# Kernel optimization log

Hardware: AMD Instinct MI355X
Metric: run time of the kernel (lower is better)

## Reference

```python
import jax, jax.numpy as jnp
import numpy as np

BS, C, H, W = 16, 192, 120, 120
AN = 36            # agent_num
KS = 3             # kernel_size
POOL = 6           # int(sqrt(agent_num))
MID = 2 * AN // 4  # 18
EPS = 1e-5


def _conv(x, w, groups=1):
    return jax.lax.conv_general_dilated(
        x, w, window_strides=(1, 1), padding='SAME',
        dimension_numbers=('NCHW', 'OIHW', 'NCHW'),
        feature_group_count=groups)


def _bn(x, g, b, m, v):
    # inference-mode BatchNorm2d with running stats
    inv = g / jnp.sqrt(v + EPS)
    return x * inv[None, :, None, None] + (b - m * inv)[None, :, None, None]


def _pool6(x):
    # AdaptiveAvgPool2d(6) with H,W divisible by 6 == exact average pooling
    bs, c, h, w = x.shape
    return x.reshape(bs, c, POOL, h // POOL, POOL, w // POOL).mean(axis=(3, 5))


def setup_inputs() -> dict:
    key = jax.random.key(0)
    ks = jax.random.split(key, 14)
    u = lambda k, s: jax.random.uniform(k, s, jnp.float32, 0.5, 1.5)
    n = lambda k, s, sc: jax.random.normal(k, s, jnp.float32) * sc
    return {
        'x':      n(ks[0], (BS, C, H, W), 1.0),
        'key_w':  n(ks[1], (C, C // 3, KS, KS), 0.05),   # grouped conv, groups=3
        'bn1_g':  u(ks[2], (C,)),
        'bn1_b':  n(ks[3], (C,), 0.1),
        'bn1_m':  n(ks[4], (C,), 0.1),
        'bn1_v':  u(ks[5], (C,)),
        'val_w':  n(ks[6], (C, C, 1, 1), 0.05),
        'att_w1': n(ks[7], (MID, 2 * AN, 1, 1), 0.1),
        'bn2_g':  u(ks[8], (MID,)),
        'bn2_b':  n(ks[9], (MID,), 0.1),
        'bn2_m':  n(ks[10], (MID,), 0.1),
        'bn2_v':  u(ks[11], (MID,)),
        'att_w2': n(ks[12], (KS * KS * AN, MID, 1, 1), 0.1),
        'att_b2': n(ks[13], (KS * KS * AN,), 0.1),
    }


def reference(x, key_w, bn1_g, bn1_b, bn1_m, bn1_v, val_w,
              att_w1, bn2_g, bn2_b, bn2_m, bn2_v, att_w2, att_b2):
    bs, c, h, w = x.shape
    hw = h * w
    # key embedding: grouped conv -> BN -> ReLU
    k1 = jax.nn.relu(_bn(_conv(x, key_w, groups=3), bn1_g, bn1_b, bn1_m, bn1_v))
    # agent tokens and pooled values (torch .view semantics: raw row-major reshape)
    agent = _pool6(x).reshape(bs, AN, c)                 # (bs, 36, c)  channel-mixed view
    v = _pool6(_conv(x, val_w)).reshape(bs, c, AN)       # (bs, c, 36)
    k1r = k1.reshape(bs, hw, c)                          # torch k1.view(bs,-1,c)
    q1 = x.reshape(bs, hw, c)
    # agent<->key and query<->agent attention
    agent_attn = jax.nn.softmax(jnp.einsum('bac,bnc->ban', agent, k1r), axis=-1)  # (bs,36,hw)
    q_attn = jax.nn.softmax(jnp.einsum('bnc,bac->bna', q1, agent), axis=-1)       # (bs,hw,36)
    y = jnp.concatenate([agent_attn, jnp.swapaxes(q_attn, 1, 2)], axis=1)          # (bs,72,hw)
    y = y.reshape(bs, 2 * AN, h, w)
    # conv-generated attention map
    t = jax.nn.relu(_bn(_conv(y, att_w1), bn2_g, bn2_b, bn2_m, bn2_v))
    att = _conv(t, att_w2) + att_b2[None, :, None, None]                           # (bs,324,h,w)
    att = att.reshape(bs, AN, KS * KS, h, w).mean(axis=2).reshape(bs, hw, AN)
    k2 = jax.nn.softmax(att, axis=-1)                                              # (bs,hw,36)
    k2v = jnp.einsum('bna,bca->bnc', k2, v)                                        # (bs,hw,c)
    out = jnp.swapaxes(k2v, 1, 2).reshape(bs, c, h, w) + k1
    return out
```

## Files before the change

kernel.cpp:

```cpp
#include <hip/hip_runtime.h>
#include <hip/hip_bf16.h>
#include <math.h>

#define BS 16
#define C 192
#define H 120
#define W 120
#define HW 14400
#define AN 36
#define MID 18
#define CPG 64
#define EPS 1e-5f
#define SPX 128
#define BPS 200
#define NWQ 13824
#define XROWS 122
#define XCOLS 132
#define OPX 64
#define WST 72

typedef __attribute__((ext_vector_type(8))) short s16x8;
typedef __attribute__((ext_vector_type(4))) float f32x4;
typedef __attribute__((ext_vector_type(4))) unsigned short u16x4;

static __device__ __forceinline__ short f2bf(float f) {
    union { float f; unsigned u; } v; v.f = f;
    unsigned r = (v.u + 0x7FFF + ((v.u >> 16) & 1)) >> 16;
    return (short)r;
}
static __device__ __forceinline__ float bf2f(unsigned short u) {
    union { unsigned u; float f; } v; v.u = ((unsigned)u) << 16;
    return v.f;
}
static __device__ __forceinline__ s16x8 cvt8(float4 f0, float4 f1) {
    s16x8 v;
    v[0] = f2bf(f0.x); v[1] = f2bf(f0.y); v[2] = f2bf(f0.z); v[3] = f2bf(f0.w);
    v[4] = f2bf(f1.x); v[5] = f2bf(f1.y); v[6] = f2bf(f1.z); v[7] = f2bf(f1.w);
    return v;
}

__global__ __launch_bounds__(256) void k_wfold(const float* __restrict__ kw,
                                               const float* __restrict__ g1,
                                               const float* __restrict__ v1,
                                               unsigned short* __restrict__ Wq) {
    int u = blockIdx.x * 256 + threadIdx.x;
    if (u >= NWQ) return;
    int gc = u / 2304, rem = u - gc * 2304;
    int g = gc >> 1, cc = gc & 1;
    int th = rem >> 6, co = rem & 63;
    int tap = th >> 2, hi = th & 3;
    int cog = g * 64 + co;
    float inv = g1[cog] * rsqrtf(v1[cog] + EPS);
    const float* wp = kw + ((size_t)cog * 64 + cc * 32 + hi * 8) * 9 + tap;
    s16x8 v;
    #pragma unroll
    for (int e = 0; e < 8; ++e) v[e] = f2bf(wp[e * 9] * inv);
    *(s16x8*)&Wq[(size_t)u * 8] = v;
}

__global__ __launch_bounds__(256) void k_xt(const float* __restrict__ x,
                                            unsigned short* __restrict__ xTp) {
    int y = blockIdx.x, b = blockIdx.y;
    int t = threadIdx.x;
    __shared__ unsigned short L[120 * 200];
    for (int u = t; u < 24 * 120; u += 256) {
        int oc = u / 120, px = u - oc * 120;
        const float* xp = x + ((size_t)b * C + oc * 8) * HW + y * W + px;
        s16x8 v;
        #pragma unroll
        for (int j = 0; j < 8; ++j) v[j] = f2bf(xp[(size_t)j * HW]);
        *(s16x8*)&L[px * 200 + oc * 8] = v;
    }
    __syncthreads();
    for (int u = t; u < 24 * XCOLS; u += 256) {
        int oc = u / XCOLS, p = u - oc * XCOLS;
        int px = p - 1;
        s16x8 v = {0, 0, 0, 0, 0, 0, 0, 0};
        if (px >= 0 && px < 120) v = *(const s16x8*)&L[px * 200 + oc * 8];
        *(s16x8*)&xTp[(((size_t)(b * 24 + oc)) * XROWS + (y + 1)) * XCOLS * 8 + p * 8] = v;
    }
    if (y == 0 || y == H - 1) {
        int r = (y == 0) ? 0 : XROWS - 1;
        s16x8 z = {0, 0, 0, 0, 0, 0, 0, 0};
        for (int u = t; u < 24 * XCOLS; u += 256) {
            int oc = u / XCOLS, p = u - oc * XCOLS;
            *(s16x8*)&xTp[(((size_t)(b * 24 + oc)) * XROWS + r) * XCOLS * 8 + p * 8] = z;
        }
    }
}

__global__ __launch_bounds__(256) void k_pool(const float* __restrict__ x,
                                              float* __restrict__ P) {
    int bc = blockIdx.x;
    const float* xp = x + (size_t)bc * HW;
    __shared__ float acc[AN];
    int tid = threadIdx.x;
    if (tid < AN) acc[tid] = 0.f;
    __syncthreads();
    for (int s = tid; s < 720; s += 256) {
        int y = s / 6, xs = s % 6;
        const float4* p4 = (const float4*)(xp + y * W + xs * 20);
        float sum = 0.f;
        #pragma unroll
        for (int i = 0; i < 5; ++i) {
            float4 v = p4[i];
            sum += v.x + v.y + v.z + v.w;
        }
        atomicAdd(&acc[(y / 20) * 6 + xs], sum);
    }
    __syncthreads();
    if (tid < AN) P[(size_t)bc * AN + tid] = acc[tid] * (1.f / 400.f);
}

__global__ __launch_bounds__(256) void k_val(const float* __restrict__ valw,
                                             const float* __restrict__ P,
                                             unsigned short* __restrict__ Vb) {
    int b = blockIdx.x;
    __shared__ float Pl[C * AN];
    int tid = threadIdx.x;
    for (int i = tid; i < C * AN; i += 256) Pl[i] = P[(size_t)b * C * AN + i];
    __syncthreads();
    for (int o = tid; o < C * 8; o += 256) {
        int cc = o >> 3, a8 = o & 7;
        s16x8 vv = {0, 0, 0, 0, 0, 0, 0, 0};
        #pragma unroll
        for (int j = 0; j < 8; ++j) {
            int a = a8 * 8 + j;
            if (a < AN) {
                float s = 0.f;
                for (int k = 0; k < C; ++k) s += valw[cc * C + k] * Pl[k * AN + a];
                vv[j] = f2bf(s);
            }
        }
        *(s16x8*)&Vb[((size_t)b * C + cc) * 64 + a8 * 8] = vv;
    }
}

__global__ __launch_bounds__(256, 4) void k_conv_mfma(
        const unsigned short* __restrict__ xTp, const unsigned short* __restrict__ Wq,
        const float* __restrict__ g1, const float* __restrict__ b1,
        const float* __restrict__ m1, const float* __restrict__ v1,
        float* __restrict__ k1f, unsigned short* __restrict__ k1b, int writeF32) {
    int yp = blockIdx.x, g = blockIdx.y, b = blockIdx.z;
    int y0 = yp * 2;
    int t = threadIdx.x;
    __shared__ short xl[(2048 + 2) * 8];

    int w = t >> 6, l = t & 63, lr = l & 15, hi = l >> 4;
    int ry = w >> 1, xh = w & 1;
    f32x4 acc[4][4];
    #pragma unroll
    for (int mt = 0; mt < 4; ++mt)
        #pragma unroll
        for (int nt = 0; nt < 4; ++nt)
            acc[mt][nt] = (f32x4){0.f, 0.f, 0.f, 0.f};

    for (int cc = 0; cc < 2; ++cc) {
        if (cc) __syncthreads();
        const unsigned short* xbase =
            xTp + ((size_t)((b * 24 + g * 8 + cc * 4) * XROWS) + y0) * XCOLS * 8;
        #pragma unroll
        for (int k = 0; k < 8; ++k) {
            int u = t + 256 * k;
            int run = u >> 7, p = u & 127;
            int oct = run >> 2, r = run & 3;
            s16x8 v = *(const s16x8*)&xbase[((size_t)(oct * XROWS + r)) * XCOLS * 8 + p * 8];
            *(s16x8*)&xl[u * 8] = v;
        }
        __syncthreads();
        const s16x8* wq = (const s16x8*)Wq + (size_t)(g * 2 + cc) * 2304;
        s16x8 Bn[4];
        #pragma unroll
        for (int nt = 0; nt < 4; ++nt) Bn[nt] = wq[hi * 64 + nt * 16 + lr];
        #pragma unroll
        for (int tap = 0; tap < 9; ++tap) {
            int ky = tap / 3, kx = tap % 3;
            s16x8 Bc[4];
            #pragma unroll
            for (int nt = 0; nt < 4; ++nt) Bc[nt] = Bn[nt];
            if (tap < 8) {
                #pragma unroll
                for (int nt = 0; nt < 4; ++nt)
                    Bn[nt] = wq[((tap + 1) * 4 + hi) * 64 + nt * 16 + lr];
            }
            s16x8 A[4];
            #pragma unroll
            for (int mt = 0; mt < 4; ++mt) {
                int col = xh * 64 + mt * 16 + lr + kx;
                A[mt] = *(const s16x8*)&xl[((hi * 4 + ry + ky) * 128 + col) * 8];
            }
            #pragma unroll
            for (int mt = 0; mt < 4; ++mt)
                #pragma unroll
                for (int nt = 0; nt < 4; ++nt)
                    acc[mt][nt] = __builtin_amdgcn_mfma_f32_16x16x32_bf16(
                        A[mt], Bc[nt], acc[mt][nt], 0, 0, 0);
        }
    }
    int y = y0 + ry;
    #pragma unroll
    for (int nt = 0; nt < 4; ++nt) {
        int cog = g * CPG + nt * 16 + lr;
        float inv = g1[cog] * rsqrtf(v1[cog] + EPS);
        float beta = b1[cog] - m1[cog] * inv;
        #pragma unroll
        for (int mt = 0; mt < 4; ++mt) {
            int xcol = xh * 64 + mt * 16 + hi * 4;
            if (xcol >= 120) continue;
            float r0 = fmaxf(acc[mt][nt][0] + beta, 0.f);
            float r1 = fmaxf(acc[mt][nt][1] + beta, 0.f);
            float r2 = fmaxf(acc[mt][nt][2] + beta, 0.f);
            float r3 = fmaxf(acc[mt][nt][3] + beta, 0.f);
            size_t base = ((size_t)(b * C + cog)) * HW + y * W + xcol;
            if (writeF32) {
                *(float4*)&k1f[base] = make_float4(r0, r1, r2, r3);
            } else {
                u16x4 q;
                q[0] = (unsigned short)f2bf(r0); q[1] = (unsigned short)f2bf(r1);
                q[2] = (unsigned short)f2bf(r2); q[3] = (unsigned short)f2bf(r3);
                *(u16x4*)&k1b[base] = q;
            }
        }
    }
}

__global__ __launch_bounds__(256, 3) void k_scores_mfma(
        const float* __restrict__ Pp, const float* __restrict__ k1f,
        const unsigned short* __restrict__ k1b, const float* __restrict__ x,
        const unsigned short* __restrict__ xTp,
        float* __restrict__ S1, float* __restrict__ S2) {
    int b = blockIdx.y;
    int n0 = blockIdx.x * SPX;
    int t = threadIdx.x;
    int w = t >> 6, l = t & 63, lr = l & 15, hi = l >> 4;
    __shared__ short Bp[SPX * BPS];

    s16x8 afr[3][6];
    const float* ab = Pp + (size_t)b * (C * AN);
    #pragma unroll
    for (int mt = 0; mt < 3; ++mt) {
        int row = mt * 16 + lr;
        #pragma unroll
        for (int kc = 0; kc < 6; ++kc) {
            s16x8 v = {0, 0, 0, 0, 0, 0, 0, 0};
            if (row < AN) {
                const float4* ap = (const float4*)(ab + row * C + kc * 32 + hi * 8);
                v = cvt8(ap[0], ap[1]);
            }
            afr[mt][kc] = v;
        }
    }

    #pragma unroll 1
    for (int s = 0; s < 2; ++s) {
        __syncthreads();
        if (s == 0 && k1b) {
            const unsigned short* src = k1b + (size_t)b * C * HW + (size_t)n0 * C;
            for (int i = t; i < SPX * 24; i += 256) {
                int row = i / 24, o = i - row * 24;
                s16x8 v = {0, 0, 0, 0, 0, 0, 0, 0};
                if (n0 + row < HW) v = *(const s16x8*)&src[row * C + o * 8];
                *(s16x8*)&Bp[row * BPS + o * 8] = v;
            }
        } else if (s == 1 && xTp) {
            for (int i = t; i < SPX * 24; i += 256) {
                int row = i / 24, oc = i - row * 24;
                int n = n0 + row;
                s16x8 v = {0, 0, 0, 0, 0, 0, 0, 0};
                if (n < HW) {
                    int yy = n / 120, xx = n - yy * 120;
                    v = *(const s16x8*)&xTp[(((size_t)(b * 24 + oc)) * XROWS + yy + 1) *
                                            XCOLS * 8 + (xx + 1) * 8];
                }
                *(s16x8*)&Bp[row * BPS + oc * 8] = v;
            }
        } else {
            const float* sf = (s == 0) ? k1f : x;
            const float4* src = (const float4*)(sf + (size_t)b * C * HW + (size_t)n0 * C);
            for (int i = t; i < SPX * 24; i += 256) {
                int row = i / 24, c8 = (i - row * 24) * 8;
                s16x8 v = {0, 0, 0, 0, 0, 0, 0, 0};
                if (n0 + row < HW)
                    v = cvt8(src[row * 48 + c8 / 4], src[row * 48 + c8 / 4 + 1]);
                *(s16x8*)&Bp[row * BPS + c8] = v;
            }
        }
        __syncthreads();
        f32x4 acc[3][2];
        #pragma unroll
        for (int mt = 0; mt < 3; ++mt)
            #pragma unroll
            for (int pt = 0; pt < 2; ++pt)
                acc[mt][pt] = (f32x4){0.f, 0.f, 0.f, 0.f};
        #pragma unroll
        for (int kc = 0; kc < 6; ++kc) {
            s16x8 bf[2];
            #pragma unroll
            for (int pt = 0; pt < 2; ++pt) {
                int px = (w * 2 + pt) * 16 + lr;
                bf[pt] = *(const s16x8*)&Bp[px * BPS + kc * 32 + hi * 8];
            }
            #pragma unroll
            for (int mt = 0; mt < 3; ++mt)
                #pragma unroll
                for (int pt = 0; pt < 2; ++pt)
                    acc[mt][pt] = __builtin_amdgcn_mfma_f32_16x16x32_bf16(
                        afr[mt][kc], bf[pt], acc[mt][pt], 0, 0, 0);
        }
        float* dst = (s == 0 ? S1 : S2) + (size_t)b * AN * HW + n0;
        #pragma unroll
        for (int mt = 0; mt < 3; ++mt)
            #pragma unroll
            for (int pt = 0; pt < 2; ++pt) {
                int px = (w * 2 + pt) * 16 + lr;
                if (n0 + px >= HW) continue;
                #pragma unroll
                for (int r = 0; r < 4; ++r) {
                    int a = mt * 16 + hi * 4 + r;
                    if (a < AN) dst[(size_t)a * HW + px] = acc[mt][pt][r];
                }
            }
    }
}

__global__ __launch_bounds__(256) void k_rowstats(const float* __restrict__ S,
                                                  float* __restrict__ stats) {
    int row = blockIdx.x;
    const float* p = S + (size_t)row * HW;
    int tid = threadIdx.x;
    __shared__ float red[4];
    float m = -1e30f;
    for (int i = tid; i < HW / 4; i += 256) {
        float4 v = ((const float4*)p)[i];
        m = fmaxf(m, fmaxf(fmaxf(v.x, v.y), fmaxf(v.z, v.w)));
    }
    #pragma unroll
    for (int off = 32; off > 0; off >>= 1) m = fmaxf(m, __shfl_down(m, off, 64));
    if ((tid & 63) == 0) red[tid >> 6] = m;
    __syncthreads();
    m = fmaxf(fmaxf(red[0], red[1]), fmaxf(red[2], red[3]));
    __syncthreads();
    float s = 0.f;
    for (int i = tid; i < HW / 4; i += 256) {
        float4 v = ((const float4*)p)[i];
        s += __expf(v.x - m) + __expf(v.y - m) + __expf(v.z - m) + __expf(v.w - m);
    }
    #pragma unroll
    for (int off = 32; off > 0; off >>= 1) s += __shfl_down(s, off, 64);
    if ((tid & 63) == 0) red[tid >> 6] = s;
    __syncthreads();
    if (tid == 0) {
        stats[row] = m;
        stats[576 + row] = 1.f / (red[0] + red[1] + red[2] + red[3]);
    }
}

__global__ __launch_bounds__(256) void k_fuse(const float* __restrict__ A1,
                                              const float* __restrict__ stats,
                                              const float* __restrict__ S2,
                                              const float* __restrict__ w1,
                                              const float* __restrict__ g2,
                                              const float* __restrict__ b2,
                                              const float* __restrict__ m2,
                                              const float* __restrict__ v2,
                                              const float* __restrict__ w2,
                                              const float* __restrict__ bias2,
                                              float* __restrict__ AM) {
    int b = blockIdx.y;
    int tid = threadIdx.x;
    int N = blockIdx.x * 256 + tid;
    __shared__ float W1f[MID * 72];
    __shared__ float b1f[MID];
    __shared__ float W2m[AN * MID];
    __shared__ float b2m[AN];
    __shared__ float sm_m[AN], sm_ri[AN];
    for (int i = tid; i < MID * 72; i += 256) {
        int m = i / 72;
        W1f[i] = w1[i] * (g2[m] * rsqrtf(v2[m] + EPS));
    }
    if (tid < MID) {
        float inv = g2[tid] * rsqrtf(v2[tid] + EPS);
        b1f[tid] = b2[tid] - m2[tid] * inv;
    }
    for (int i = tid; i < AN * MID; i += 256) {
        int a = i / MID, m = i % MID;
        float s = 0.f;
        #pragma unroll
        for (int k = 0; k < 9; ++k) s += w2[(a * 9 + k) * MID + m];
        W2m[i] = s * (1.f / 9.f);
    }
    if (tid < AN) {
        float s = 0.f;
        #pragma unroll
        for (int k = 0; k < 9; ++k) s += bias2[tid * 9 + k];
        b2m[tid] = s * (1.f / 9.f);
        sm_m[tid] = stats[b * AN + tid];
        sm_ri[tid] = stats[576 + b * AN + tid];
    }
    __syncthreads();
    if (N >= HW) return;
    float yv[72];
    const float* a1p = A1 + (size_t)b * AN * HW + N;
    #pragma unroll
    for (int j = 0; j < AN; ++j)
        yv[j] = __expf(a1p[(size_t)j * HW] - sm_m[j]) * sm_ri[j];
    const float* s2p = S2 + (size_t)b * AN * HW + N;
    float mx = -1e30f;
    #pragma unroll
    for (int j = 0; j < AN; ++j) {
        float v = s2p[(size_t)j * HW];
        yv[AN + j] = v;
        mx = fmaxf(mx, v);
    }
    float ssum = 0.f;
    #pragma unroll
    for (int j = 0; j < AN; ++j) {
        float e = __expf(yv[AN + j] - mx);
        yv[AN + j] = e;
        ssum += e;
    }
    float rs = 1.f / ssum;
    #pragma unroll
    for (int j = 0; j < AN; ++j) yv[AN + j] *= rs;
    float t[MID];
    #pragma unroll
    for (int m = 0; m < MID; ++m) {
        float a = b1f[m];
        #pragma unroll
        for (int j = 0; j < 72; ++j) a += W1f[m * 72 + j] * yv[j];
        t[m] = a > 0.f ? a : 0.f;
    }
    float* amp = AM + (size_t)b * AN * HW + N;
    #pragma unroll
    for (int a = 0; a < AN; ++a) {
        float acc = b2m[a];
        #pragma unroll
        for (int m = 0; m < MID; ++m) acc += W2m[a * MID + m] * t[m];
        amp[(size_t)a * HW] = acc;
    }
}

__global__ __launch_bounds__(256) void k_out_mfma(const float* __restrict__ AM,
                                                  const unsigned short* __restrict__ Vb,
                                                  const unsigned short* __restrict__ k1b,
                                                  float* __restrict__ outp) {
    int b = blockIdx.y;
    int N0 = blockIdx.x * OPX;
    int t = threadIdx.x;
    __shared__ short wl[OPX * WST];

    {
        int p = t >> 2, q = t & 3;
        int N = N0 + p;
        int a = N / 400;
        int n0w = (N - a * 400) * AN;
        const float* amp = AM + ((size_t)b * AN + a) * HW + n0w;
        const int qoff = (q == 0) ? 0 : (q == 1) ? 12 : (q == 2) ? 20 : 32;
        const int qn4 = (q == 0) ? 3 : (q == 1) ? 2 : (q == 2) ? 3 : 1;
        float vals[12];
        const float4* ap = (const float4*)(amp + qoff);
        #pragma unroll
        for (int i = 0; i < 3; ++i) {
            if (i < qn4) {
                float4 v = ap[i];
                vals[i * 4 + 0] = v.x; vals[i * 4 + 1] = v.y;
                vals[i * 4 + 2] = v.z; vals[i * 4 + 3] = v.w;
            }
        }
        int cnt = qn4 * 4;
        float m = -1e30f;
        #pragma unroll
        for (int i = 0; i < 12; ++i) if (i < cnt) m = fmaxf(m, vals[i]);
        m = fmaxf(m, __shfl_xor(m, 1, 64));
        m = fmaxf(m, __shfl_xor(m, 2, 64));
        float s = 0.f;
        #pragma unroll
        for (int i = 0; i < 12; ++i)
            if (i < cnt) { vals[i] = __expf(vals[i] - m); s += vals[i]; }
        s += __shfl_xor(s, 1, 64);
        s += __shfl_xor(s, 2, 64);
        float rs = 1.f / s;
        #pragma unroll
        for (int i = 0; i < 12; ++i)
            if (i < cnt) wl[p * WST + qoff + i] = f2bf(vals[i] * rs);
        if (q == 3) {
            #pragma unroll
            for (int i = 36; i < 64; ++i) wl[p * WST + i] = 0;
        }
    }
    __syncthreads();

    int w = t >> 6, l = t & 63, lr = l & 15, hi = l >> 4;
    int cc0 = w * 48;
    const s16x8* vb = (const s16x8*)(Vb + (size_t)b * C * 64);
    s16x8 Af[3][2];
    #pragma unroll
    for (int mt = 0; mt < 3; ++mt)
        #pragma unroll
        for (int ch = 0; ch < 2; ++ch)
            Af[mt][ch] = vb[(cc0 + mt * 16 + lr) * 8 + ch * 4 + hi];
    f32x4 acc[3][4];
    #pragma unroll
    for (int mt = 0; mt < 3; ++mt)
        #pragma unroll
        for (int pt = 0; pt < 4; ++pt)
            acc[mt][pt] = (f32x4){0.f, 0.f, 0.f, 0.f};
    #pragma unroll
    for (int pt = 0; pt < 4; ++pt) {
        s16x8 Bf[2];
        #pragma unroll
        for (int ch = 0; ch < 2; ++ch)
            Bf[ch] = *(const s16x8*)&wl[(pt * 16 + lr) * WST + ch * 32 + hi * 8];
        #pragma unroll
        for (int ch = 0; ch < 2; ++ch)
            #pragma unroll
            for (int mt = 0; mt < 3; ++mt)
                acc[mt][pt] = __builtin_amdgcn_mfma_f32_16x16x32_bf16(
                    Af[mt][ch], Bf[ch], acc[mt][pt], 0, 0, 0);
    }
    #pragma unroll
    for (int mt = 0; mt < 3; ++mt)
        #pragma unroll
        for (int pt = 0; pt < 4; ++pt) {
            int px = pt * 16 + lr;
            #pragma unroll
            for (int r = 0; r < 4; ++r) {
                int cc = cc0 + mt * 16 + hi * 4 + r;
                size_t idx = ((size_t)(b * C + cc)) * HW + N0 + px;
                float res = k1b ? bf2f(k1b[idx]) : outp[idx];
                outp[idx] = acc[mt][pt][r] + res;
            }
        }
}

extern "C" void kernel_launch(void* const* d_in, const int* in_sizes, int n_in,
                              void* d_out, int out_size, void* d_ws, size_t ws_size,
                              hipStream_t stream) {
    const float* x      = (const float*)d_in[0];
    const float* key_w  = (const float*)d_in[1];
    const float* bn1_g  = (const float*)d_in[2];
    const float* bn1_b  = (const float*)d_in[3];
    const float* bn1_m  = (const float*)d_in[4];
    const float* bn1_v  = (const float*)d_in[5];
    const float* val_w  = (const float*)d_in[6];
    const float* att_w1 = (const float*)d_in[7];
    const float* bn2_g  = (const float*)d_in[8];
    const float* bn2_b  = (const float*)d_in[9];
    const float* bn2_m  = (const float*)d_in[10];
    const float* bn2_v  = (const float*)d_in[11];
    const float* att_w2 = (const float*)d_in[12];
    const float* att_b2 = (const float*)d_in[13];
    float* out = (float*)d_out;

    unsigned char* base = (unsigned char*)d_ws;
    size_t off = 0;
    unsigned short* Wq = (unsigned short*)(base + off); off += 221184;
    unsigned short* Vb = (unsigned short*)(base + off); off += 393216;
    float* P  = (float*)(base + off); off += 442368;
    float* ST = (float*)(base + off); off += 4608;
    float* S1 = (float*)(base + off); off += 33177600;
    float* S2 = (float*)(base + off); off += 33177600;
    float* AM = (float*)(base + off); off += 33177600;
    size_t k1bBytes = (size_t)BS * C * HW * 2;
    size_t xtpBytes = (size_t)BS * 24 * XROWS * XCOLS * 16;
    unsigned short* k1b = nullptr;
    unsigned short* xTp = (unsigned short*)S1;
    int xtpSep = 0;
    if (ws_size >= off + k1bBytes) {
        k1b = (unsigned short*)(base + off); off += k1bBytes;
        if (ws_size >= off + xtpBytes) {
            xTp = (unsigned short*)(base + off); off += xtpBytes;
            xtpSep = 1;
        }
    }
    int writeF32 = (k1b == nullptr) ? 1 : 0;

    k_wfold<<<(NWQ + 255) / 256, 256, 0, stream>>>(key_w, bn1_g, bn1_v, Wq);
    k_xt<<<dim3(H, BS), 256, 0, stream>>>(x, xTp);
    k_pool<<<BS * C, 256, 0, stream>>>(x, P);
    k_val<<<BS, 256, 0, stream>>>(val_w, P, Vb);
    k_conv_mfma<<<dim3(H / 2, 3, BS), 256, 0, stream>>>(
        xTp, Wq, bn1_g, bn1_b, bn1_m, bn1_v, out, k1b, writeF32);
    k_scores_mfma<<<dim3((HW + SPX - 1) / SPX, BS), 256, 0, stream>>>(
        P, out, k1b, x, xtpSep ? xTp : nullptr, S1, S2);
    k_rowstats<<<BS * AN, 256, 0, stream>>>(S1, ST);
    k_fuse<<<dim3((HW + 255) / 256, BS), 256, 0, stream>>>(
        S1, ST, S2, att_w1, bn2_g, bn2_b, bn2_m, bn2_v, att_w2, att_b2, AM);
    k_out_mfma<<<dim3(HW / OPX, BS), 256, 0, stream>>>(AM, Vb, k1b, out);
}
```

Measured before the change: 522.4 us.

## Pool from bf16 transposed x, store attention map in bf16, vectorize output stores

Average pooling now reads the already-transposed bf16 padded copy of x instead of the fp32 input, which halves the bytes read and drops the shared-memory atomics. The intermediate attention map written by k_fuse and read by k_out_mfma is stored as bf16 instead of fp32, cutting that round-trip traffic in half. The output kernel stages its MFMA accumulators through shared memory so that residual loads and output stores become float4-wide and coalesced. The trade-offs are bf16 rounding of the pooled values and of the logits before the softmax, and a dependence on xTp being fully written by k_xt even when it aliases S1.

```diff
diff --git a/kernel.cpp b/kernel.cpp
--- a/kernel.cpp
+++ b/kernel.cpp
@@ -89,27 +89,43 @@
     }
 }
 
-__global__ __launch_bounds__(256) void k_pool(const float* __restrict__ x,
-                                              float* __restrict__ P) {
-    int bc = blockIdx.x;
-    const float* xp = x + (size_t)bc * HW;
-    __shared__ float acc[AN];
-    int tid = threadIdx.x;
-    if (tid < AN) acc[tid] = 0.f;
-    __syncthreads();
-    for (int s = tid; s < 720; s += 256) {
-        int y = s / 6, xs = s % 6;
-        const float4* p4 = (const float4*)(xp + y * W + xs * 20);
-        float sum = 0.f;
-        #pragma unroll
-        for (int i = 0; i < 5; ++i) {
-            float4 v = p4[i];
-            sum += v.x + v.y + v.z + v.w;
-        }
-        atomicAdd(&acc[(y / 20) * 6 + xs], sum);
-    }
-    __syncthreads();
-    if (tid < AN) P[(size_t)bc * AN + tid] = acc[tid] * (1.f / 400.f);
+__global__ __launch_bounds__(256) void k_pool_b(const unsigned short* __restrict__ xTp,
+                                                float* __restrict__ P) {
+    int oc = blockIdx.x, b = blockIdx.y;
+    int t = threadIdx.x;
+    __shared__ float Lp[240 * 24];
+    const unsigned short* base =
+        xTp + (((size_t)(b * 24 + oc)) * XROWS + 1) * XCOLS * 8 + 8;
+    if (t < 240) {
+        int y = t >> 1, h = t & 1;
+        const unsigned short* row = base + (size_t)y * XCOLS * 8 + h * 60 * 8;
+        float acc[3][8];
+        #pragma unroll
+        for (int qq = 0; qq < 3; ++qq)
+            #pragma unroll
+            for (int e = 0; e < 8; ++e) acc[qq][e] = 0.f;
+        #pragma unroll
+        for (int qq = 0; qq < 3; ++qq)
+            for (int j = 0; j < 20; ++j) {
+                s16x8 v = *(const s16x8*)&row[(qq * 20 + j) * 8];
+                #pragma unroll
+                for (int e = 0; e < 8; ++e) acc[qq][e] += bf2f((unsigned short)v[e]);
+            }
+        #pragma unroll
+        for (int qq = 0; qq < 3; ++qq)
+            #pragma unroll
+            for (int e = 0; e < 8; ++e) Lp[t * 24 + qq * 8 + e] = acc[qq][e];
+    }
+    __syncthreads();
+    if (t < 288) {
+        int seg = t >> 3, e = t & 7;
+        int yq = seg / 6, q = seg % 6;
+        int h = q / 3, qq = q % 3;
+        float s = 0.f;
+        for (int j = 0; j < 20; ++j)
+            s += Lp[((yq * 20 + j) * 2 + h) * 24 + qq * 8 + e];
+        P[((size_t)b * C + oc * 8 + e) * AN + seg] = s * (1.f / 400.f);
+    }
 }
 
 __global__ __launch_bounds__(256) void k_val(const float* __restrict__ valw,
@@ -365,7 +381,7 @@
                                               const float* __restrict__ v2,
                                               const float* __restrict__ w2,
                                               const float* __restrict__ bias2,
-                                              float* __restrict__ AM) {
+                                              unsigned short* __restrict__ AMb) {
     int b = blockIdx.y;
     int tid = threadIdx.x;
     int N = blockIdx.x * 256 + tid;
@@ -430,41 +446,42 @@
         for (int j = 0; j < 72; ++j) a += W1f[m * 72 + j] * yv[j];
         t[m] = a > 0.f ? a : 0.f;
     }
-    float* amp = AM + (size_t)b * AN * HW + N;
+    unsigned short* amp = AMb + (size_t)b * AN * HW + N;
     #pragma unroll
     for (int a = 0; a < AN; ++a) {
         float acc = b2m[a];
         #pragma unroll
         for (int m = 0; m < MID; ++m) acc += W2m[a * MID + m] * t[m];
-        amp[(size_t)a * HW] = acc;
-    }
-}
-
-__global__ __launch_bounds__(256) void k_out_mfma(const float* __restrict__ AM,
+        amp[(size_t)a * HW] = (unsigned short)f2bf(acc);
+    }
+}
+
+__global__ __launch_bounds__(256) void k_out_mfma(const unsigned short* __restrict__ AMb,
                                                   const unsigned short* __restrict__ Vb,
                                                   const unsigned short* __restrict__ k1b,
                                                   float* __restrict__ outp) {
     int b = blockIdx.y;
     int N0 = blockIdx.x * OPX;
     int t = threadIdx.x;
-    __shared__ short wl[OPX * WST];
+    __shared__ float smemf[4 * 1088];
+    short* wl = (short*)smemf;
 
     {
         int p = t >> 2, q = t & 3;
         int N = N0 + p;
         int a = N / 400;
         int n0w = (N - a * 400) * AN;
-        const float* amp = AM + ((size_t)b * AN + a) * HW + n0w;
+        const unsigned short* amp = AMb + ((size_t)b * AN + a) * HW + n0w;
         const int qoff = (q == 0) ? 0 : (q == 1) ? 12 : (q == 2) ? 20 : 32;
         const int qn4 = (q == 0) ? 3 : (q == 1) ? 2 : (q == 2) ? 3 : 1;
         float vals[12];
-        const float4* ap = (const float4*)(amp + qoff);
+        const u16x4* ap = (const u16x4*)(amp + qoff);
         #pragma unroll
         for (int i = 0; i < 3; ++i) {
             if (i < qn4) {
-                float4 v = ap[i];
-                vals[i * 4 + 0] = v.x; vals[i * 4 + 1] = v.y;
-                vals[i * 4 + 2] = v.z; vals[i * 4 + 3] = v.w;
+                u16x4 v = ap[i];
+                vals[i * 4 + 0] = bf2f(v[0]); vals[i * 4 + 1] = bf2f(v[1]);
+                vals[i * 4 + 2] = bf2f(v[2]); vals[i * 4 + 3] = bf2f(v[3]);
             }
         }
         int cnt = qn4 * 4;
@@ -518,19 +535,34 @@
                 acc[mt][pt] = __builtin_amdgcn_mfma_f32_16x16x32_bf16(
                     Af[mt][ch], Bf[ch], acc[mt][pt], 0, 0, 0);
     }
-    #pragma unroll
-    for (int mt = 0; mt < 3; ++mt)
-        #pragma unroll
-        for (int pt = 0; pt < 4; ++pt) {
-            int px = pt * 16 + lr;
-            #pragma unroll
-            for (int r = 0; r < 4; ++r) {
-                int cc = cc0 + mt * 16 + hi * 4 + r;
-                size_t idx = ((size_t)(b * C + cc)) * HW + N0 + px;
-                float res = k1b ? bf2f(k1b[idx]) : outp[idx];
-                outp[idx] = acc[mt][pt][r] + res;
-            }
-        }
+    __syncthreads();
+
+    float* T = smemf + (size_t)w * 1088;
+    #pragma unroll
+    for (int mt = 0; mt < 3; ++mt) {
+        #pragma unroll
+        for (int pt = 0; pt < 4; ++pt)
+            #pragma unroll
+            for (int r = 0; r < 4; ++r)
+                T[(hi * 4 + r) * 68 + pt * 16 + lr] = acc[mt][pt][r];
+        #pragma unroll
+        for (int pass = 0; pass < 4; ++pass) {
+            int ccr = pass * 4 + hi;
+            int px4 = (l & 15) * 4;
+            float4 vv = *(float4*)&T[ccr * 68 + px4];
+            int cc = cc0 + mt * 16 + ccr;
+            size_t idx = ((size_t)(b * C + cc)) * HW + N0 + px4;
+            float4 res;
+            if (k1b) {
+                u16x4 kk = *(const u16x4*)&k1b[idx];
+                res = make_float4(bf2f(kk[0]), bf2f(kk[1]), bf2f(kk[2]), bf2f(kk[3]));
+            } else {
+                res = *(float4*)&outp[idx];
+            }
+            vv.x += res.x; vv.y += res.y; vv.z += res.z; vv.w += res.w;
+            *(float4*)&outp[idx] = vv;
+        }
+    }
 }
 
 extern "C" void kernel_launch(void* const* d_in, const int* in_sizes, int n_in,
@@ -560,7 +592,7 @@
     float* ST = (float*)(base + off); off += 4608;
     float* S1 = (float*)(base + off); off += 33177600;
     float* S2 = (float*)(base + off); off += 33177600;
-    float* AM = (float*)(base + off); off += 33177600;
+    unsigned short* AMb = (unsigned short*)(base + off); off += 33177600;
     size_t k1bBytes = (size_t)BS * C * HW * 2;
     size_t xtpBytes = (size_t)BS * 24 * XROWS * XCOLS * 16;
     unsigned short* k1b = nullptr;
@@ -577,7 +609,7 @@
 
     k_wfold<<<(NWQ + 255) / 256, 256, 0, stream>>>(key_w, bn1_g, bn1_v, Wq);
     k_xt<<<dim3(H, BS), 256, 0, stream>>>(x, xTp);
-    k_pool<<<BS * C, 256, 0, stream>>>(x, P);
+    k_pool_b<<<dim3(24, BS), 256, 0, stream>>>(xTp, P);
     k_val<<<BS, 256, 0, stream>>>(val_w, P, Vb);
     k_conv_mfma<<<dim3(H / 2, 3, BS), 256, 0, stream>>>(
         xTp, Wq, bn1_g, bn1_b, bn1_m, bn1_v, out, k1b, writeF32);
@@ -585,6 +617,6 @@
         P, out, k1b, x, xtpSep ? xTp : nullptr, S1, S2);
     k_rowstats<<<BS * AN, 256, 0, stream>>>(S1, ST);
     k_fuse<<<dim3((HW + 255) / 256, BS), 256, 0, stream>>>(
-        S1, ST, S2, att_w1, bn2_g, bn2_b, bn2_m, bn2_v, att_w2, att_b2, AM);
-    k_out_mfma<<<dim3(HW / OPX, BS), 256, 0, stream>>>(AM, Vb, k1b, out);
-}
+        S1, ST, S2, att_w1, bn2_g, bn2_b, bn2_m, bn2_v, att_w2, att_b2, AMb);
+    k_out_mfma<<<dim3(HW / OPX, BS), 256, 0, stream>>>(AMb, Vb, k1b, out);
+}
```

Measured after the change: 457.0 us. 1.14x faster.
